# Optimization experiments

Hardware: AMD Instinct MI355X
Metric: run time of the kernel (lower is better)

The kernel has to match this reference:

```python
import jax, jax.numpy as jnp
import numpy as np

B, IN_DIM, HID, ATT = 16384, 128, 512, 256
TOTAL = IN_DIM + HID + ATT


def setup_inputs() -> dict:
    key = jax.random.key(0)
    ks = jax.random.split(key, 10)
    u = lambda k, shape, lo, hi: jax.random.uniform(k, shape, jnp.float32, lo, hi)
    return {
        "t": jnp.float32(0.0),
        "h_ltc": jax.random.normal(ks[0], (B, HID), jnp.float32),
        "x_t": jax.random.normal(ks[1], (B, IN_DIM), jnp.float32),
        "context": jax.random.normal(ks[2], (B, ATT), jnp.float32),
        "W_gd": u(ks[3], (2 * HID, TOTAL), -0.1, 0.1),
        "b_gd": u(ks[4], (2 * HID,), -0.1, 0.1),
        "W_tau": u(ks[5], (HID, HID), -0.1, 0.1),
        "b_tau": u(ks[6], (HID,), -0.1, 0.1),
        "gleak": u(ks[7], (HID,), 0.001, 1.0),
        "cm": u(ks[8], (HID,), 0.4, 0.6),
    }


def reference(t, h_ltc, x_t, context, W_gd, b_gd, W_tau, b_tau, gleak, cm):
    # combined: [B, IN+HID+ATT]
    combined = jnp.concatenate([x_t, h_ltc, context], axis=1)
    g_d = combined @ W_gd.T + b_gd            # [B, 2*HID]
    gate, dynamics = jnp.split(g_d, 2, axis=1)
    tau = jax.nn.softplus(h_ltc @ W_tau.T + b_tau)  # [B, HID]
    numerator = jax.nn.sigmoid(gate) * jnp.tanh(dynamics) - h_ltc
    denominator = tau + jax.nn.softplus(cm) + jax.nn.softplus(gleak)
    return numerator / (denominator + 1e-6)
```

## Files before the change

### kernel.cpp

```cpp
#include <hip/hip_runtime.h>
#include <hip/hip_bf16.h>
#include <math.h>

#define BROWS 16384
#define IN_DIM 128
#define HID 512
#define ATT 256
#define KTOT 896
#define KC_TOT 112

typedef __bf16 bf16x8 __attribute__((ext_vector_type(8)));
typedef float f32x4 __attribute__((ext_vector_type(4)));

__device__ __forceinline__ float softplus_f(float x) {
    return fmaxf(x, 0.0f) + log1pf(__expf(-fabsf(x)));
}

__global__ void pack_B(const float* __restrict__ W_gd, const float* __restrict__ W_tau,
                       const float* __restrict__ gleak, const float* __restrict__ cm,
                       __hip_bfloat16* __restrict__ B_stage, float* __restrict__ dconst) {
    const int cid = blockIdx.x * 256 + threadIdx.x;
    if (cid < HID) {
        dconst[cid] = softplus_f(cm[cid]) + softplus_f(gleak[cid]) + 1e-6f;
    }
    const int nl = cid % 192;
    const int kc = (cid / 192) % KC_TOT;
    const int jt = cid / (192 * KC_TOT);
    const int jg = nl / 48, type = (nl % 48) / 16, j16 = nl % 16;
    const int j = jt * 64 + jg * 16 + j16;
    const int k0 = kc * 8;

    float v[8];
    if (type == 0) {
        const float* s = W_gd + (size_t)j * KTOT + k0;
        #pragma unroll
        for (int i = 0; i < 8; ++i) v[i] = s[i];
    } else if (type == 1) {
        const float* s = W_gd + (size_t)(HID + j) * KTOT + k0;
        #pragma unroll
        for (int i = 0; i < 8; ++i) v[i] = s[i];
    } else {
        if (k0 >= IN_DIM && k0 < IN_DIM + HID) {
            const float* s = W_tau + (size_t)j * HID + (k0 - IN_DIM);
            #pragma unroll
            for (int i = 0; i < 8; ++i) v[i] = s[i];
        } else {
            #pragma unroll
            for (int i = 0; i < 8; ++i) v[i] = 0.0f;
        }
    }
    union { __hip_bfloat16 hh[8]; uint4 u; } p;
    #pragma unroll
    for (int i = 0; i < 8; ++i) p.hh[i] = __float2bfloat16(v[i]);
    *(uint4*)(B_stage + (size_t)cid * 8) = p.u;
}

__device__ __forceinline__ void slab_src(int ks, const float* x, const float* h,
                                         const float* c, const float*& src,
                                         int& rs, int& c0) {
    if (ks < 2)       { src = x; rs = IN_DIM; c0 = ks * 64; }
    else if (ks < 10) { src = h; rs = HID;    c0 = (ks - 2) * 64; }
    else              { src = c; rs = ATT;    c0 = (ks - 10) * 64; }
}

__global__ __launch_bounds__(256, 2) void ltc_gemm(
    const float* __restrict__ x, const float* __restrict__ h_ltc,
    const float* __restrict__ ctx, const __hip_bfloat16* __restrict__ B_stage,
    const float* __restrict__ b_gd, const float* __restrict__ b_tau,
    const float* __restrict__ dconst, float* __restrict__ out) {

    __shared__ __attribute__((aligned(16))) char smem[16384 + 24576];
    char* As = smem;
    char* Bs = smem + 16384;

    const int bx = blockIdx.x;
    const int mt = bx & 127;
    const int jt = bx >> 7;
    const int tid = threadIdx.x;
    const int wave = tid >> 6, lane = tid & 63;
    const int wm = wave >> 1;
    const int wj = wave & 1;
    const int q = lane >> 4, t = lane & 15;

    const int kc8 = tid & 7;
    const int mi0 = tid >> 3;

    f32x4 accg[2][4], accd[2][4], acct[2][4];
    #pragma unroll
    for (int g = 0; g < 2; ++g)
        #pragma unroll
        for (int i = 0; i < 4; ++i) {
            accg[g][i] = (f32x4)0.0f; accd[g][i] = (f32x4)0.0f; acct[g][i] = (f32x4)0.0f;
        }

    const __hip_bfloat16* bSrc[6]; char* bDst[6];
    #pragma unroll
    for (int r = 0; r < 6; ++r) {
        int c = wave + 4 * r;
        bSrc[r] = B_stage + (size_t)jt * (KC_TOT * 1536) + c * 512 + lane * 8;
        bDst[r] = Bs + c * 1024;
    }

    float4 pf[4][2];
    {
        const float* src; int rs, c0;
        slab_src(0, x, h_ltc, ctx, src, rs, c0);
        #pragma unroll
        for (int r = 0; r < 4; ++r) {
            const float* p = src + (size_t)(mt * 128 + mi0 + 32 * r) * rs + c0 + kc8 * 8;
            pf[r][0] = *(const float4*)p;
            pf[r][1] = *(const float4*)(p + 4);
        }
    }

    for (int ks = 0; ks < 14; ++ks) {
        #pragma unroll
        for (int r = 0; r < 4; ++r) {
            union { __hip_bfloat16 hh[8]; uint4 u; } pk;
            pk.hh[0] = __float2bfloat16(pf[r][0].x);
            pk.hh[1] = __float2bfloat16(pf[r][0].y);
            pk.hh[2] = __float2bfloat16(pf[r][0].z);
            pk.hh[3] = __float2bfloat16(pf[r][0].w);
            pk.hh[4] = __float2bfloat16(pf[r][1].x);
            pk.hh[5] = __float2bfloat16(pf[r][1].y);
            pk.hh[6] = __float2bfloat16(pf[r][1].z);
            pk.hh[7] = __float2bfloat16(pf[r][1].w);
            const int mi = mi0 + 32 * r;
            *(uint4*)(As + ((kc8 * 128 + (mi ^ kc8)) << 4)) = pk.u;
        }
        #pragma unroll
        for (int r = 0; r < 6; ++r)
            __builtin_amdgcn_global_load_lds(
                (const __attribute__((address_space(1))) void*)bSrc[r],
                (__attribute__((address_space(3))) void*)bDst[r], 16, 0, 0);
        __syncthreads();

        if (ks < 13) {
            const float* src; int rs, c0;
            slab_src(ks + 1, x, h_ltc, ctx, src, rs, c0);
            #pragma unroll
            for (int r = 0; r < 4; ++r) {
                const float* p = src + (size_t)(mt * 128 + mi0 + 32 * r) * rs + c0 + kc8 * 8;
                pf[r][0] = *(const float4*)p;
                pf[r][1] = *(const float4*)(p + 4);
            }
        }

        const bool tau_on = (ks >= 2 && ks < 10);
        #pragma unroll
        for (int ko2 = 0; ko2 < 2; ++ko2) {
            const int kcl = ko2 * 4 + q;
            const char* ab = As + ((kcl * 128 + ((wm * 64 + t) ^ kcl)) << 4);
            bf16x8 a0 = *(const bf16x8*)(ab);
            bf16x8 a1 = *(const bf16x8*)(ab + 256);
            bf16x8 a2 = *(const bf16x8*)(ab + 512);
            bf16x8 a3 = *(const bf16x8*)(ab + 768);
            #pragma unroll
            for (int g = 0; g < 2; ++g) {
                const char* bb = Bs + (((kcl * 192) + wj * 96 + g * 48 + t) << 4);
                bf16x8 bg = *(const bf16x8*)(bb);
                bf16x8 bd = *(const bf16x8*)(bb + 256);
                accg[g][0] = __builtin_amdgcn_mfma_f32_16x16x32_bf16(a0, bg, accg[g][0], 0, 0, 0);
                accg[g][1] = __builtin_amdgcn_mfma_f32_16x16x32_bf16(a1, bg, accg[g][1], 0, 0, 0);
                accg[g][2] = __builtin_amdgcn_mfma_f32_16x16x32_bf16(a2, bg, accg[g][2], 0, 0, 0);
                accg[g][3] = __builtin_amdgcn_mfma_f32_16x16x32_bf16(a3, bg, accg[g][3], 0, 0, 0);
                accd[g][0] = __builtin_amdgcn_mfma_f32_16x16x32_bf16(a0, bd, accd[g][0], 0, 0, 0);
                accd[g][1] = __builtin_amdgcn_mfma_f32_16x16x32_bf16(a1, bd, accd[g][1], 0, 0, 0);
                accd[g][2] = __builtin_amdgcn_mfma_f32_16x16x32_bf16(a2, bd, accd[g][2], 0, 0, 0);
                accd[g][3] = __builtin_amdgcn_mfma_f32_16x16x32_bf16(a3, bd, accd[g][3], 0, 0, 0);
                if (tau_on) {
                    bf16x8 bt = *(const bf16x8*)(bb + 512);
                    acct[g][0] = __builtin_amdgcn_mfma_f32_16x16x32_bf16(a0, bt, acct[g][0], 0, 0, 0);
                    acct[g][1] = __builtin_amdgcn_mfma_f32_16x16x32_bf16(a1, bt, acct[g][1], 0, 0, 0);
                    acct[g][2] = __builtin_amdgcn_mfma_f32_16x16x32_bf16(a2, bt, acct[g][2], 0, 0, 0);
                    acct[g][3] = __builtin_amdgcn_mfma_f32_16x16x32_bf16(a3, bt, acct[g][3], 0, 0, 0);
                }
            }
        }
        #pragma unroll
        for (int r = 0; r < 6; ++r) bSrc[r] += 12288;
        __syncthreads();
    }

    const int row0 = mt * 128 + wm * 64 + q * 4;
    #pragma unroll
    for (int g = 0; g < 2; ++g) {
        const int j = jt * 64 + (wj * 2 + g) * 16 + t;
        const float bgj = b_gd[j];
        const float bdj = b_gd[HID + j];
        const float btj = b_tau[j];
        const float dcj = dconst[j];
        #pragma unroll
        for (int i = 0; i < 4; ++i) {
            #pragma unroll
            for (int r = 0; r < 4; ++r) {
                const int row = row0 + i * 16 + r;
                const float gv = accg[g][i][r] + bgj;
                const float dv = accd[g][i][r] + bdj;
                const float tp = acct[g][i][r] + btj;
                const float hv = h_ltc[(size_t)row * HID + j];
                const float sig = __builtin_amdgcn_rcpf(1.0f + __expf(-gv));
                const float th  = 1.0f - 2.0f * __builtin_amdgcn_rcpf(__expf(2.0f * dv) + 1.0f);
                const float tau = fmaxf(tp, 0.0f) + __logf(1.0f + __expf(-fabsf(tp)));
                out[(size_t)row * HID + j] = (sig * th - hv) * __builtin_amdgcn_rcpf(tau + dcj);
            }
        }
    }
}

extern "C" void kernel_launch(void* const* d_in, const int* in_sizes, int n_in,
                              void* d_out, int out_size, void* d_ws, size_t ws_size,
                              hipStream_t stream) {
    const float* h_ltc = (const float*)d_in[1];
    const float* x_t   = (const float*)d_in[2];
    const float* ctx   = (const float*)d_in[3];
    const float* W_gd  = (const float*)d_in[4];
    const float* b_gd  = (const float*)d_in[5];
    const float* W_tau = (const float*)d_in[6];
    const float* b_tau = (const float*)d_in[7];
    const float* gleak = (const float*)d_in[8];
    const float* cm    = (const float*)d_in[9];

    char* ws = (char*)d_ws;
    __hip_bfloat16* B_stage = (__hip_bfloat16*)ws;
    float* dconst = (float*)(ws + 2752512);

    pack_B<<<672, 256, 0, stream>>>(W_gd, W_tau, gleak, cm, B_stage, dconst);
    ltc_gemm<<<1024, 256, 0, stream>>>(x_t, h_ltc, ctx, B_stage, b_gd, b_tau, dconst,
                                       (float*)d_out);
}
```

Before: 170.2 us.

## Use 512-thread blocks with 8 waves, one N-subtile per wave

New measurement: 169.0 us. Within noise of the previous version (-0.7%).

```diff
diff --git a/kernel.cpp b/kernel.cpp
--- a/kernel.cpp
+++ b/kernel.cpp
@@ -63,7 +63,7 @@
     else              { src = c; rs = ATT;    c0 = (ks - 10) * 64; }
 }
 
-__global__ __launch_bounds__(256, 2) void ltc_gemm(
+__global__ __launch_bounds__(512, 4) void ltc_gemm(
     const float* __restrict__ x, const float* __restrict__ h_ltc,
     const float* __restrict__ ctx, const __hip_bfloat16* __restrict__ B_stage,
     const float* __restrict__ b_gd, const float* __restrict__ b_tau,
@@ -78,36 +78,34 @@
     const int jt = bx >> 7;
     const int tid = threadIdx.x;
     const int wave = tid >> 6, lane = tid & 63;
-    const int wm = wave >> 1;
-    const int wj = wave & 1;
+    const int wm = wave >> 2;
+    const int wj = wave & 3;
     const int q = lane >> 4, t = lane & 15;
 
     const int kc8 = tid & 7;
     const int mi0 = tid >> 3;
 
-    f32x4 accg[2][4], accd[2][4], acct[2][4];
-    #pragma unroll
-    for (int g = 0; g < 2; ++g)
-        #pragma unroll
-        for (int i = 0; i < 4; ++i) {
-            accg[g][i] = (f32x4)0.0f; accd[g][i] = (f32x4)0.0f; acct[g][i] = (f32x4)0.0f;
-        }
-
-    const __hip_bfloat16* bSrc[6]; char* bDst[6];
-    #pragma unroll
-    for (int r = 0; r < 6; ++r) {
-        int c = wave + 4 * r;
+    f32x4 accg[4], accd[4], acct[4];
+    #pragma unroll
+    for (int i = 0; i < 4; ++i) {
+        accg[i] = (f32x4)0.0f; accd[i] = (f32x4)0.0f; acct[i] = (f32x4)0.0f;
+    }
+
+    const __hip_bfloat16* bSrc[3]; char* bDst[3];
+    #pragma unroll
+    for (int r = 0; r < 3; ++r) {
+        int c = wave + 8 * r;
         bSrc[r] = B_stage + (size_t)jt * (KC_TOT * 1536) + c * 512 + lane * 8;
         bDst[r] = Bs + c * 1024;
     }
 
-    float4 pf[4][2];
+    float4 pf[2][2];
     {
         const float* src; int rs, c0;
         slab_src(0, x, h_ltc, ctx, src, rs, c0);
         #pragma unroll
-        for (int r = 0; r < 4; ++r) {
-            const float* p = src + (size_t)(mt * 128 + mi0 + 32 * r) * rs + c0 + kc8 * 8;
+        for (int r = 0; r < 2; ++r) {
+            const float* p = src + (size_t)(mt * 128 + mi0 + 64 * r) * rs + c0 + kc8 * 8;
             pf[r][0] = *(const float4*)p;
             pf[r][1] = *(const float4*)(p + 4);
         }
@@ -115,7 +113,12 @@
 
     for (int ks = 0; ks < 14; ++ks) {
         #pragma unroll
-        for (int r = 0; r < 4; ++r) {
+        for (int r = 0; r < 3; ++r)
+            __builtin_amdgcn_global_load_lds(
+                (const __attribute__((address_space(1))) void*)bSrc[r],
+                (__attribute__((address_space(3))) void*)bDst[r], 16, 0, 0);
+        #pragma unroll
+        for (int r = 0; r < 2; ++r) {
             union { __hip_bfloat16 hh[8]; uint4 u; } pk;
             pk.hh[0] = __float2bfloat16(pf[r][0].x);
             pk.hh[1] = __float2bfloat16(pf[r][0].y);
@@ -125,22 +128,17 @@
             pk.hh[5] = __float2bfloat16(pf[r][1].y);
             pk.hh[6] = __float2bfloat16(pf[r][1].z);
             pk.hh[7] = __float2bfloat16(pf[r][1].w);
-            const int mi = mi0 + 32 * r;
+            const int mi = mi0 + 64 * r;
             *(uint4*)(As + ((kc8 * 128 + (mi ^ kc8)) << 4)) = pk.u;
         }
-        #pragma unroll
-        for (int r = 0; r < 6; ++r)
-            __builtin_amdgcn_global_load_lds(
-                (const __attribute__((address_space(1))) void*)bSrc[r],
-                (__attribute__((address_space(3))) void*)bDst[r], 16, 0, 0);
         __syncthreads();
 
         if (ks < 13) {
             const float* src; int rs, c0;
             slab_src(ks + 1, x, h_ltc, ctx, src, rs, c0);
             #pragma unroll
-            for (int r = 0; r < 4; ++r) {
-                const float* p = src + (size_t)(mt * 128 + mi0 + 32 * r) * rs + c0 + kc8 * 8;
+            for (int r = 0; r < 2; ++r) {
+                const float* p = src + (size_t)(mt * 128 + mi0 + 64 * r) * rs + c0 + kc8 * 8;
                 pf[r][0] = *(const float4*)p;
                 pf[r][1] = *(const float4*)(p + 4);
             }
@@ -155,55 +153,49 @@
             bf16x8 a1 = *(const bf16x8*)(ab + 256);
             bf16x8 a2 = *(const bf16x8*)(ab + 512);
             bf16x8 a3 = *(const bf16x8*)(ab + 768);
-            #pragma unroll
-            for (int g = 0; g < 2; ++g) {
-                const char* bb = Bs + (((kcl * 192) + wj * 96 + g * 48 + t) << 4);
-                bf16x8 bg = *(const bf16x8*)(bb);
-                bf16x8 bd = *(const bf16x8*)(bb + 256);
-                accg[g][0] = __builtin_amdgcn_mfma_f32_16x16x32_bf16(a0, bg, accg[g][0], 0, 0, 0);
-                accg[g][1] = __builtin_amdgcn_mfma_f32_16x16x32_bf16(a1, bg, accg[g][1], 0, 0, 0);
-                accg[g][2] = __builtin_amdgcn_mfma_f32_16x16x32_bf16(a2, bg, accg[g][2], 0, 0, 0);
-                accg[g][3] = __builtin_amdgcn_mfma_f32_16x16x32_bf16(a3, bg, accg[g][3], 0, 0, 0);
-                accd[g][0] = __builtin_amdgcn_mfma_f32_16x16x32_bf16(a0, bd, accd[g][0], 0, 0, 0);
-                accd[g][1] = __builtin_amdgcn_mfma_f32_16x16x32_bf16(a1, bd, accd[g][1], 0, 0, 0);
-                accd[g][2] = __builtin_amdgcn_mfma_f32_16x16x32_bf16(a2, bd, accd[g][2], 0, 0, 0);
-                accd[g][3] = __builtin_amdgcn_mfma_f32_16x16x32_bf16(a3, bd, accd[g][3], 0, 0, 0);
-                if (tau_on) {
-                    bf16x8 bt = *(const bf16x8*)(bb + 512);
-                    acct[g][0] = __builtin_amdgcn_mfma_f32_16x16x32_bf16(a0, bt, acct[g][0], 0, 0, 0);
-                    acct[g][1] = __builtin_amdgcn_mfma_f32_16x16x32_bf16(a1, bt, acct[g][1], 0, 0, 0);
-                    acct[g][2] = __builtin_amdgcn_mfma_f32_16x16x32_bf16(a2, bt, acct[g][2], 0, 0, 0);
-                    acct[g][3] = __builtin_amdgcn_mfma_f32_16x16x32_bf16(a3, bt, acct[g][3], 0, 0, 0);
-                }
+            const char* bb = Bs + (((kcl * 192) + wj * 48 + t) << 4);
+            bf16x8 bg = *(const bf16x8*)(bb);
+            bf16x8 bd = *(const bf16x8*)(bb + 256);
+            accg[0] = __builtin_amdgcn_mfma_f32_16x16x32_bf16(a0, bg, accg[0], 0, 0, 0);
+            accg[1] = __builtin_amdgcn_mfma_f32_16x16x32_bf16(a1, bg, accg[1], 0, 0, 0);
+            accg[2] = __builtin_amdgcn_mfma_f32_16x16x32_bf16(a2, bg, accg[2], 0, 0, 0);
+            accg[3] = __builtin_amdgcn_mfma_f32_16x16x32_bf16(a3, bg, accg[3], 0, 0, 0);
+            accd[0] = __builtin_amdgcn_mfma_f32_16x16x32_bf16(a0, bd, accd[0], 0, 0, 0);
+            accd[1] = __builtin_amdgcn_mfma_f32_16x16x32_bf16(a1, bd, accd[1], 0, 0, 0);
+            accd[2] = __builtin_amdgcn_mfma_f32_16x16x32_bf16(a2, bd, accd[2], 0, 0, 0);
+            accd[3] = __builtin_amdgcn_mfma_f32_16x16x32_bf16(a3, bd, accd[3], 0, 0, 0);
+            if (tau_on) {
+                bf16x8 bt = *(const bf16x8*)(bb + 512);
+                acct[0] = __builtin_amdgcn_mfma_f32_16x16x32_bf16(a0, bt, acct[0], 0, 0, 0);
+                acct[1] = __builtin_amdgcn_mfma_f32_16x16x32_bf16(a1, bt, acct[1], 0, 0, 0);
+                acct[2] = __builtin_amdgcn_mfma_f32_16x16x32_bf16(a2, bt, acct[2], 0, 0, 0);
+                acct[3] = __builtin_amdgcn_mfma_f32_16x16x32_bf16(a3, bt, acct[3], 0, 0, 0);
             }
         }
         #pragma unroll
-        for (int r = 0; r < 6; ++r) bSrc[r] += 12288;
+        for (int r = 0; r < 3; ++r) bSrc[r] += 12288;
         __syncthreads();
     }
 
     const int row0 = mt * 128 + wm * 64 + q * 4;
-    #pragma unroll
-    for (int g = 0; g < 2; ++g) {
-        const int j = jt * 64 + (wj * 2 + g) * 16 + t;
-        const float bgj = b_gd[j];
-        const float bdj = b_gd[HID + j];
-        const float btj = b_tau[j];
-        const float dcj = dconst[j];
-        #pragma unroll
-        for (int i = 0; i < 4; ++i) {
-            #pragma unroll
-            for (int r = 0; r < 4; ++r) {
-                const int row = row0 + i * 16 + r;
-                const float gv = accg[g][i][r] + bgj;
-                const float dv = accd[g][i][r] + bdj;
-                const float tp = acct[g][i][r] + btj;
-                const float hv = h_ltc[(size_t)row * HID + j];
-                const float sig = __builtin_amdgcn_rcpf(1.0f + __expf(-gv));
-                const float th  = 1.0f - 2.0f * __builtin_amdgcn_rcpf(__expf(2.0f * dv) + 1.0f);
-                const float tau = fmaxf(tp, 0.0f) + __logf(1.0f + __expf(-fabsf(tp)));
-                out[(size_t)row * HID + j] = (sig * th - hv) * __builtin_amdgcn_rcpf(tau + dcj);
-            }
+    const int j = jt * 64 + wj * 16 + t;
+    const float bgj = b_gd[j];
+    const float bdj = b_gd[HID + j];
+    const float btj = b_tau[j];
+    const float dcj = dconst[j];
+    #pragma unroll
+    for (int i = 0; i < 4; ++i) {
+        #pragma unroll
+        for (int r = 0; r < 4; ++r) {
+            const int row = row0 + i * 16 + r;
+            const float gv = accg[i][r] + bgj;
+            const float dv = accd[i][r] + bdj;
+            const float tp = acct[i][r] + btj;
+            const float hv = h_ltc[(size_t)row * HID + j];
+            const float sig = __builtin_amdgcn_rcpf(1.0f + __expf(-gv));
+            const float th  = 1.0f - 2.0f * __builtin_amdgcn_rcpf(__expf(2.0f * dv) + 1.0f);
+            const float tau = fmaxf(tp, 0.0f) + __logf(1.0f + __expf(-fabsf(tp)));
+            out[(size_t)row * HID + j] = (sig * th - hv) * __builtin_amdgcn_rcpf(tau + dcj);
         }
     }
 }
@@ -226,6 +218,6 @@
     float* dconst = (float*)(ws + 2752512);
 
     pack_B<<<672, 256, 0, stream>>>(W_gd, W_tau, gleak, cm, B_stage, dconst);
-    ltc_gemm<<<1024, 256, 0, stream>>>(x_t, h_ltc, ctx, B_stage, b_gd, b_tau, dconst,
+    ltc_gemm<<<1024, 512, 0, stream>>>(x_t, h_ltc, ctx, B_stage, b_gd, b_tau, dconst,
                                        (float*)d_out);
 }
```
